# Optimization experiments

Measured on AMD Instinct MI355X. Metric: run time of the kernel, lower is better.

The kernel has to match this reference:

```python
import jax, jax.numpy as jnp
import numpy as np

K_BINS = 16   # radial bins
O_BINS = 8    # angular bins


def setup_inputs() -> dict:
    key = jax.random.key(0)
    k1, k2 = jax.random.split(key, 2)
    x = jax.random.normal(k1, (64, 3, 512, 512), dtype=jnp.float32)
    W = jax.random.normal(k2, (64, 24), dtype=jnp.float32) * 0.1  # Linear(K+O=24 -> proj=64) weight
    b = jnp.zeros((64,), dtype=jnp.float32)
    return {"x": x, "W": W, "b": b}


def _spectrum_hist(x):
    B = x.shape[0]
    # rfft2 magnitude, averaged over channels: [B, H2, W2]
    spec = jnp.abs(jnp.fft.rfft2(x, norm="ortho")).mean(axis=1)
    H2, W2 = spec.shape[-2], spec.shape[-1]
    yy, xx = jnp.meshgrid(
        jnp.linspace(-1.0, 1.0, H2, dtype=jnp.float32),
        jnp.linspace(0.0, 1.0, W2, dtype=jnp.float32),
        indexing="ij",
    )
    rr = jnp.clip(jnp.sqrt(yy * yy + xx * xx), 0.0, 1.0 - 1e-8)
    th = jnp.arctan2(yy, xx + 1e-9) + jnp.pi / 2
    rb = jnp.clip((rr * K_BINS).astype(jnp.int32), 0, K_BINS - 1).reshape(-1)
    ob = jnp.clip((th / jnp.pi * O_BINS).astype(jnp.int32), 0, O_BINS - 1).reshape(-1)
    mag = jnp.log1p(spec).reshape(B, -1)  # [B, H2*W2]
    rad = jax.vmap(lambda m: jax.ops.segment_sum(m, rb, num_segments=K_BINS))(mag)
    ang = jax.vmap(lambda m: jax.ops.segment_sum(m, ob, num_segments=O_BINS))(mag)
    rad = rad / (rad.sum(-1, keepdims=True) + 1e-6)
    ang = ang / (ang.sum(-1, keepdims=True) + 1e-6)
    return jnp.concatenate([rad, ang], axis=1)  # [B, K+O]


def reference(x, W, b):
    h = _spectrum_hist(x.astype(jnp.float32))
    return h @ W.T + b  # [B, proj]
```

## Files before the change

### kernel.cpp

```cpp
#include <hip/hip_runtime.h>
#include <math.h>


#define TPB0 256
#define TPB1 1024
#define TPB2 256
#define W2 257
#define NTILE 65
#define CS 529
#define CSU (2*CS)
#define CSB 513
#define FTS 512
#define PI_F 3.14159265358979323846f
#define TWO_PI_F 6.28318530717958647692f
#define SB() __builtin_amdgcn_sched_barrier(0)
#define PH(i) ((i) ^ ((((i) >> 6) & 7) * 9))

static constexpr float TW32_RE[16] = {
   1.0f,          0.98078528f,  0.92387953f,  0.83146961f,
   0.70710678f,   0.55557023f,  0.38268343f,  0.19509032f,
   0.0f,         -0.19509032f, -0.38268343f, -0.55557023f,
  -0.70710678f,  -0.83146961f, -0.92387953f, -0.98078528f };
static constexpr float TW32_IM[16] = {
  -0.0f,         -0.19509032f, -0.38268343f, -0.55557023f,
  -0.70710678f,  -0.83146961f, -0.92387953f, -0.98078528f,
  -1.0f,         -0.98078528f, -0.92387953f, -0.83146961f,
  -0.70710678f,  -0.55557023f, -0.38268343f, -0.19509032f };

static constexpr int BR3[8] = {0,4,2,6,1,5,3,7};

__device__ __forceinline__ float2 cmulf(float2 a, float2 b) {
  return make_float2(a.x*b.x - a.y*b.y, a.x*b.y + a.y*b.x);
}
__device__ __forceinline__ unsigned bfpack(float2 v) {
  unsigned a = __float_as_uint(v.x) >> 16;
  unsigned b = __float_as_uint(v.y) & 0xFFFF0000u;
  return b | a;
}
__device__ __forceinline__ float2 bfunpack(unsigned p) {
  return make_float2(__uint_as_float(p << 16), __uint_as_float(p & 0xFFFF0000u));
}

template <int LOGN>
__device__ __forceinline__ void fft_reg(float2* z) {
  const int N = 1 << LOGN;
  #pragma unroll
  for (int s = 0; s < LOGN; ++s) {
    const int h = 1 << s;
    #pragma unroll
    for (int g0 = 0; g0 < N; g0 += 2 * h) {
      #pragma unroll
      for (int jj = 0; jj < h; ++jj) {
        const int k = jj << (4 - s);
        const float wr = TW32_RE[k], wi = TW32_IM[k];
        float2 a = z[g0 + jj];
        float2 b = z[g0 + jj + h];
        float tr = b.x * wr - b.y * wi;
        float ti = b.x * wi + b.y * wr;
        z[g0 + jj]     = make_float2(a.x + tr, a.y + ti);
        z[g0 + jj + h] = make_float2(a.x - tr, a.y - ti);
      }
    }
  }
}

__device__ __forceinline__ void twiddle_chain(float2* z, float2 base) {
  float2 wk = base;
  #pragma unroll
  for (int k = 1; k < 8; ++k) {
    z[k] = cmulf(z[k], wk);
    if (k < 7) wk = cmulf(wk, base);
  }
}

__device__ __forceinline__ void get_bins(int i, int j, int& rb, int& ob) {
  float yy = -1.0f + (float)i * (2.0f / 511.0f);
  float xx = (float)j * (1.0f / 256.0f);
  float rr = sqrtf(yy * yy + xx * xx);
  rr = fminf(rr, 1.0f - 1e-8f);
  float th = atan2f(yy, xx + 1e-9f) + 1.57079632679489662f;
  rb = (int)(rr * 16.0f);
  rb = rb < 0 ? 0 : (rb > 15 ? 15 : rb);
  ob = (int)((th / PI_F) * 8.0f);
  ob = ob < 0 ? 0 : (ob > 7 ? 7 : ob);
}

__global__ __launch_bounds__(TPB0) void pass0_kernel(unsigned char* __restrict__ binsT) {
  int j = blockIdx.x;
  #pragma unroll
  for (int e = 0; e < 2; e++) {
    int i = threadIdx.x + e * 256;
    int rb, ob;
    get_bins(i, j, rb, ob);
    binsT[(size_t)j * 512 + i] = (unsigned char)(rb | (ob << 4));
  }
}

__global__ __launch_bounds__(TPB1, 4) void pass1_kernel(
    const float* __restrict__ x, unsigned* __restrict__ FT, int ic0) {
  __shared__ float2 xbuf[16 * CS];
  int t = threadIdx.x;
  int segblk = blockIdx.x & 15;
  int ic_local = blockIdx.x >> 4;
  int wv = t >> 6;
  int u = t & 63;
  int rp = segblk * 16 + wv;
  const float* row0 = x + (((size_t)(ic0 + ic_local)) * 512 + (size_t)rp * 2) * 512;
  const float* row1 = row0 + 512;
  float2* seg = xbuf + wv * CS;
  unsigned* useg = (unsigned*)xbuf + wv * CSU;

  const int ul = u & 7, wq = u >> 3;
  const int x9 = 9 * wq, b64 = 64 * wq;

  float2 w1, w64;
  { float sn, cs;
    sincosf(-TWO_PI_F * (float)u * (1.0f / 512.0f), &sn, &cs);  w1  = make_float2(cs, sn);
    sincosf(-TWO_PI_F * (float)ul * (1.0f / 64.0f), &sn, &cs);  w64 = make_float2(cs, sn); }

  float2 z[8];
  #pragma unroll
  for (int m = 0; m < 8; ++m)
    z[BR3[m]] = make_float2(row0[u + 64 * m], row1[u + 64 * m]);
  fft_reg<3>(z);
  twiddle_chain(z, w1);
  SB();
  #pragma unroll
  for (int k3 = 0; k3 < 8; ++k3) seg[(u ^ (9 * k3)) + 64 * k3] = z[k3];
  SB();
  #pragma unroll
  for (int g2 = 0; g2 < 8; ++g2) z[BR3[g2]] = seg[((ul + 8 * g2) ^ x9) + b64];
  fft_reg<3>(z);
  twiddle_chain(z, w64);
  SB();
  #pragma unroll
  for (int K2 = 0; K2 < 8; ++K2) seg[((K2 * 8 + ul) ^ x9) + b64] = z[K2];
  SB();
  #pragma unroll
  for (int gg = 0; gg < 8; ++gg) z[BR3[gg]] = seg[((ul * 8 + gg) ^ x9) + b64];
  fft_reg<3>(z);
  SB();
  #pragma unroll
  for (int K1 = 0; K1 < 8; ++K1)
    seg[((wq + 8 * ul) ^ (9 * K1)) + 64 * K1] = z[K1];
  SB();
  unsigned p0[4], p1[4];
  #pragma unroll
  for (int e = 0; e < 4; ++e) {
    int k = u + 64 * e;
    int km = (512 - k) & 511;
    float2 zk = seg[PH(k)];
    float2 zm = seg[PH(km)];
    p0[e] = bfpack(make_float2(0.5f * (zk.x + zm.x),  0.5f * (zk.y - zm.y)));
    p1[e] = bfpack(make_float2(0.5f * (zk.y + zm.y), -0.5f * (zk.x - zm.x)));
  }
  unsigned p0n = 0, p1n = 0;
  if (u == 0) {
    float2 zk = seg[PH(256)];
    p0n = bfpack(make_float2(zk.x, 0.0f));
    p1n = bfpack(make_float2(zk.y, 0.0f));
  }
  SB();
  #pragma unroll
  for (int e = 0; e < 4; ++e) {
    int k = u + 64 * e;
    useg[k] = p0[e];
    useg[257 + k] = p1[e];
  }
  if (u == 0) { useg[256] = p0n; useg[513] = p1n; }
  __syncthreads();

  unsigned* FTc = FT + (size_t)ic_local * (W2 * FTS);
  int i0 = segblk * 32;
  const unsigned* xb = (const unsigned*)xbuf;
  #pragma unroll
  for (int it = 0; it < 9; ++it) {
    int idx = t + TPB1 * it;
    if (idx < W2 * 32) {
      int j = idx >> 5;
      int il = idx & 31;
      unsigned v = xb[(il >> 1) * CSU + (il & 1) * 257 + j];
      FTc[(size_t)j * FTS + i0 + il] = v;
    }
  }
}

__global__ __launch_bounds__(TPB2, 4) void pass2_kernel(
    const unsigned* __restrict__ FT, const unsigned char* __restrict__ binsT,
    float* __restrict__ partial, int b0) {
  __shared__ unsigned xbuf[4 * CSB];
  __shared__ float hist[128];
  int t = threadIdx.x;
  int tile = blockIdx.x % NTILE;
  int b_local = blockIdx.x / NTILE;
  int wv = t >> 6;
  int u = t & 63;
  int j = tile * 4 + wv;
  bool jvalid = (j < W2);
  unsigned* seg = xbuf + wv * CSB;
  const int ul = u & 7, wq = u >> 3;
  const int x9 = 9 * wq, b64 = 64 * wq;

  if (t < 128) hist[t] = 0.0f;
  __syncthreads();

  if (jvalid) {
    float2 w1, w64;
    { float sn, cs;
      sincosf(-TWO_PI_F * (float)u * (1.0f / 512.0f), &sn, &cs);  w1  = make_float2(cs, sn);
      sincosf(-TWO_PI_F * (float)ul * (1.0f / 64.0f), &sn, &cs);  w64 = make_float2(cs, sn); }

    float mag[8];
    #pragma unroll
    for (int q = 0; q < 8; ++q) mag[q] = 0.0f;

    for (int c = 0; c < 3; ++c) {
      const unsigned* col = FT + ((size_t)(b_local * 3 + c) * W2 + j) * FTS;
      float2 z[8];
      #pragma unroll
      for (int m = 0; m < 8; ++m) z[BR3[m]] = bfunpack(col[u + 64 * m]);
      fft_reg<3>(z);
      twiddle_chain(z, w1);
      SB();
      #pragma unroll
      for (int k3 = 0; k3 < 8; ++k3) seg[(u ^ (9 * k3)) + 64 * k3] = bfpack(z[k3]);
      SB();
      #pragma unroll
      for (int g2 = 0; g2 < 8; ++g2) z[BR3[g2]] = bfunpack(seg[((ul + 8 * g2) ^ x9) + b64]);
      fft_reg<3>(z);
      twiddle_chain(z, w64);
      SB();
      #pragma unroll
      for (int K2 = 0; K2 < 8; ++K2) seg[((K2 * 8 + ul) ^ x9) + b64] = bfpack(z[K2]);
      SB();
      #pragma unroll
      for (int gg = 0; gg < 8; ++gg) z[BR3[gg]] = bfunpack(seg[((ul * 8 + gg) ^ x9) + b64]);
      fft_reg<3>(z);
      #pragma unroll
      for (int K1 = 0; K1 < 8; ++K1)
        mag[K1] += sqrtf(z[K1].x * z[K1].x + z[K1].y * z[K1].y);
      SB();
    }

    const unsigned char* bj = binsT + (size_t)j * 512;
    #pragma unroll
    for (int K1 = 0; K1 < 8; ++K1) {
      int row = wq + 8 * ul + 64 * K1;
      int code = bj[row];
      atomicAdd(&hist[code], log1pf(mag[K1] * (1.0f / 1536.0f)));
    }
  }
  __syncthreads();

  int b = b0 + b_local;
  if (t < 16) {
    float s = 0.0f;
    #pragma unroll
    for (int ob = 0; ob < 8; ++ob) s += hist[t + 16 * ob];
    partial[((size_t)b * NTILE + tile) * 24 + t] = s;
  } else if (t < 24) {
    float s = 0.0f;
    int ob = t - 16;
    #pragma unroll
    for (int rb = 0; rb < 16; ++rb) s += hist[rb + 16 * ob];
    partial[((size_t)b * NTILE + tile) * 24 + t] = s;
  }
}

__global__ __launch_bounds__(TPB0) void pass3_kernel(
    const float* __restrict__ partial, const float* __restrict__ W,
    const float* __restrict__ bias, float* __restrict__ out) {
  __shared__ float h[24];
  __shared__ float hn[24];
  int b = blockIdx.x;
  int t = threadIdx.x;
  if (t < 24) {
    float s = 0.0f;
    for (int tile = 0; tile < NTILE; tile++)
      s += partial[((size_t)b * NTILE + tile) * 24 + t];
    h[t] = s;
  }
  __syncthreads();
  if (t == 0) {
    float rs = 0.0f, as = 0.0f;
    for (int k = 0; k < 16; k++) rs += h[k];
    for (int k = 16; k < 24; k++) as += h[k];
    for (int k = 0; k < 16; k++) hn[k] = h[k] / (rs + 1e-6f);
    for (int k = 16; k < 24; k++) hn[k] = h[k] / (as + 1e-6f);
  }
  __syncthreads();
  if (t < 64) {
    float acc = bias[t];
    #pragma unroll
    for (int k = 0; k < 24; k++) acc += hn[k] * W[t * 24 + k];
    out[b * 64 + t] = acc;
  }
}

extern "C" void kernel_launch(void* const* d_in, const int* in_sizes, int n_in,
                              void* d_out, int out_size, void* d_ws, size_t ws_size,
                              hipStream_t stream) {
  const float* x    = (const float*)d_in[0];
  const float* W    = (const float*)d_in[1];
  const float* bias = (const float*)d_in[2];
  float* out = (float*)d_out;

  const size_t partial_bytes = (size_t)64 * NTILE * 24 * sizeof(float);
  size_t off_bins = (partial_bytes + 255) & ~(size_t)255;
  const size_t bins_bytes = (size_t)W2 * 512;
  size_t off_F = ((off_bins + bins_bytes) + 255) & ~(size_t)255;

  float* partial = (float*)d_ws;
  unsigned char* binsT = (unsigned char*)d_ws + off_bins;
  unsigned* FT = (unsigned*)((char*)d_ws + off_F);

  const size_t per_batch = (size_t)3 * W2 * FTS * sizeof(unsigned);
  size_t avail = ws_size > off_F ? ws_size - off_F : 0;
  int bpc = (int)(avail / per_batch);
  if (bpc < 1) bpc = 1;
  if (bpc > 64) bpc = 64;

  pass0_kernel<<<W2, TPB0, 0, stream>>>(binsT);

  for (int b0 = 0; b0 < 64; b0 += bpc) {
    int nb = (64 - b0) < bpc ? (64 - b0) : bpc;
    pass1_kernel<<<nb * 3 * 16, TPB1, 0, stream>>>(x, FT, b0 * 3);
    pass2_kernel<<<nb * NTILE, TPB2, 0, stream>>>(FT, binsT, partial, b0);
  }
  pass3_kernel<<<64, TPB0, 0, stream>>>(partial, W, bias, out);
}
```

Before: 177.2 us.

## Parallelize column FFT across channels with one wave per channel

The column-FFT pass now gives each block a single frequency column. Its three waves each handle one input channel in parallel, replacing the previous scheme where one wave looped over the three channels for one of four columns. Magnitudes go to shared memory, are summed across channels, and are binned into a block histogram. This removes the serial channel loop and the idle waves in the last tile. In exchange it adds a block barrier, a shared magnitude buffer, four times as many partial histograms, and a longer reduction in the final pass.

New measurement: 213.9 us. +20.7%, slower.

```diff
diff --git a/kernel.cpp b/kernel.cpp
--- a/kernel.cpp
+++ b/kernel.cpp
@@ -4,9 +4,8 @@
 
 #define TPB0 256
 #define TPB1 1024
-#define TPB2 256
+#define TPB2 192
 #define W2 257
-#define NTILE 65
 #define CS 529
 #define CSU (2*CS)
 #define CSB 513
@@ -188,67 +187,58 @@
 __global__ __launch_bounds__(TPB2, 4) void pass2_kernel(
     const unsigned* __restrict__ FT, const unsigned char* __restrict__ binsT,
     float* __restrict__ partial, int b0) {
-  __shared__ unsigned xbuf[4 * CSB];
+  __shared__ unsigned xseg[3 * CSB];
+  __shared__ float magbuf[3][512];
   __shared__ float hist[128];
   int t = threadIdx.x;
-  int tile = blockIdx.x % NTILE;
-  int b_local = blockIdx.x / NTILE;
-  int wv = t >> 6;
+  int j = blockIdx.x % W2;
+  int b_local = blockIdx.x / W2;
+  int c = t >> 6;
   int u = t & 63;
-  int j = tile * 4 + wv;
-  bool jvalid = (j < W2);
-  unsigned* seg = xbuf + wv * CSB;
+  unsigned* seg = xseg + c * CSB;
   const int ul = u & 7, wq = u >> 3;
   const int x9 = 9 * wq, b64 = 64 * wq;
 
   if (t < 128) hist[t] = 0.0f;
-  __syncthreads();
-
-  if (jvalid) {
-    float2 w1, w64;
-    { float sn, cs;
-      sincosf(-TWO_PI_F * (float)u * (1.0f / 512.0f), &sn, &cs);  w1  = make_float2(cs, sn);
-      sincosf(-TWO_PI_F * (float)ul * (1.0f / 64.0f), &sn, &cs);  w64 = make_float2(cs, sn); }
-
-    float mag[8];
-    #pragma unroll
-    for (int q = 0; q < 8; ++q) mag[q] = 0.0f;
-
-    for (int c = 0; c < 3; ++c) {
-      const unsigned* col = FT + ((size_t)(b_local * 3 + c) * W2 + j) * FTS;
-      float2 z[8];
-      #pragma unroll
-      for (int m = 0; m < 8; ++m) z[BR3[m]] = bfunpack(col[u + 64 * m]);
-      fft_reg<3>(z);
-      twiddle_chain(z, w1);
-      SB();
-      #pragma unroll
-      for (int k3 = 0; k3 < 8; ++k3) seg[(u ^ (9 * k3)) + 64 * k3] = bfpack(z[k3]);
-      SB();
-      #pragma unroll
-      for (int g2 = 0; g2 < 8; ++g2) z[BR3[g2]] = bfunpack(seg[((ul + 8 * g2) ^ x9) + b64]);
-      fft_reg<3>(z);
-      twiddle_chain(z, w64);
-      SB();
-      #pragma unroll
-      for (int K2 = 0; K2 < 8; ++K2) seg[((K2 * 8 + ul) ^ x9) + b64] = bfpack(z[K2]);
-      SB();
-      #pragma unroll
-      for (int gg = 0; gg < 8; ++gg) z[BR3[gg]] = bfunpack(seg[((ul * 8 + gg) ^ x9) + b64]);
-      fft_reg<3>(z);
-      #pragma unroll
-      for (int K1 = 0; K1 < 8; ++K1)
-        mag[K1] += sqrtf(z[K1].x * z[K1].x + z[K1].y * z[K1].y);
-      SB();
-    }
-
-    const unsigned char* bj = binsT + (size_t)j * 512;
-    #pragma unroll
-    for (int K1 = 0; K1 < 8; ++K1) {
-      int row = wq + 8 * ul + 64 * K1;
-      int code = bj[row];
-      atomicAdd(&hist[code], log1pf(mag[K1] * (1.0f / 1536.0f)));
-    }
+
+  float2 w1, w64;
+  { float sn, cs;
+    sincosf(-TWO_PI_F * (float)u * (1.0f / 512.0f), &sn, &cs);  w1  = make_float2(cs, sn);
+    sincosf(-TWO_PI_F * (float)ul * (1.0f / 64.0f), &sn, &cs);  w64 = make_float2(cs, sn); }
+
+  const unsigned* col = FT + ((size_t)(b_local * 3 + c) * W2 + j) * FTS;
+  float2 z[8];
+  #pragma unroll
+  for (int m = 0; m < 8; ++m) z[BR3[m]] = bfunpack(col[u + 64 * m]);
+  fft_reg<3>(z);
+  twiddle_chain(z, w1);
+  SB();
+  #pragma unroll
+  for (int k3 = 0; k3 < 8; ++k3) seg[(u ^ (9 * k3)) + 64 * k3] = bfpack(z[k3]);
+  SB();
+  #pragma unroll
+  for (int g2 = 0; g2 < 8; ++g2) z[BR3[g2]] = bfunpack(seg[((ul + 8 * g2) ^ x9) + b64]);
+  fft_reg<3>(z);
+  twiddle_chain(z, w64);
+  SB();
+  #pragma unroll
+  for (int K2 = 0; K2 < 8; ++K2) seg[((K2 * 8 + ul) ^ x9) + b64] = bfpack(z[K2]);
+  SB();
+  #pragma unroll
+  for (int gg = 0; gg < 8; ++gg) z[BR3[gg]] = bfunpack(seg[((ul * 8 + gg) ^ x9) + b64]);
+  fft_reg<3>(z);
+  #pragma unroll
+  for (int K1 = 0; K1 < 8; ++K1) {
+    int row = wq + 8 * ul + 64 * K1;
+    magbuf[c][row] = sqrtf(z[K1].x * z[K1].x + z[K1].y * z[K1].y);
+  }
+  __syncthreads();
+
+  const unsigned char* bj = binsT + (size_t)j * 512;
+  for (int row = t; row < 512; row += TPB2) {
+    float m = magbuf[0][row] + magbuf[1][row] + magbuf[2][row];
+    int code = bj[row];
+    atomicAdd(&hist[code], log1pf(m * (1.0f / 1536.0f)));
   }
   __syncthreads();
 
@@ -257,13 +247,13 @@
     float s = 0.0f;
     #pragma unroll
     for (int ob = 0; ob < 8; ++ob) s += hist[t + 16 * ob];
-    partial[((size_t)b * NTILE + tile) * 24 + t] = s;
+    partial[((size_t)b * W2 + j) * 24 + t] = s;
   } else if (t < 24) {
     float s = 0.0f;
     int ob = t - 16;
     #pragma unroll
     for (int rb = 0; rb < 16; ++rb) s += hist[rb + 16 * ob];
-    partial[((size_t)b * NTILE + tile) * 24 + t] = s;
+    partial[((size_t)b * W2 + j) * 24 + t] = s;
   }
 }
 
@@ -276,8 +266,8 @@
   int t = threadIdx.x;
   if (t < 24) {
     float s = 0.0f;
-    for (int tile = 0; tile < NTILE; tile++)
-      s += partial[((size_t)b * NTILE + tile) * 24 + t];
+    for (int jc = 0; jc < W2; jc++)
+      s += partial[((size_t)b * W2 + jc) * 24 + t];
     h[t] = s;
   }
   __syncthreads();
@@ -305,7 +295,7 @@
   const float* bias = (const float*)d_in[2];
   float* out = (float*)d_out;
 
-  const size_t partial_bytes = (size_t)64 * NTILE * 24 * sizeof(float);
+  const size_t partial_bytes = (size_t)64 * W2 * 24 * sizeof(float);
   size_t off_bins = (partial_bytes + 255) & ~(size_t)255;
   const size_t bins_bytes = (size_t)W2 * 512;
   size_t off_F = ((off_bins + bins_bytes) + 255) & ~(size_t)255;
@@ -325,7 +315,7 @@
   for (int b0 = 0; b0 < 64; b0 += bpc) {
     int nb = (64 - b0) < bpc ? (64 - b0) : bpc;
     pass1_kernel<<<nb * 3 * 16, TPB1, 0, stream>>>(x, FT, b0 * 3);
-    pass2_kernel<<<nb * NTILE, TPB2, 0, stream>>>(FT, binsT, partial, b0);
+    pass2_kernel<<<nb * W2, TPB2, 0, stream>>>(FT, binsT, partial, b0);
   }
   pass3_kernel<<<64, TPB0, 0, stream>>>(partial, W, bias, out);
 }
```
